# Kernel optimization log

Hardware: AMD Instinct MI355X
Metric: run time of the kernel (lower is better)

## Reference

```python
import jax, jax.numpy as jnp
import numpy as np

N, M = 30000, 32
VX, VY, VZ = 0.2, 0.2, 4.0
XOFF, YOFF, ZOFF = 0.1, -39.9, -1.0  # vx/2+pc_range[0], vy/2+pc_range[1], vz/2+pc_range[2]
EPS = 1e-3
H = 3  # num_heads, head_dim = 3 // 3 = 1


def setup_inputs() -> dict:
    key = jax.random.key(0)
    ks = jax.random.split(key, 13)
    features = jax.random.normal(ks[0], (N, M, 4), jnp.float32)
    num_points = jax.random.randint(ks[1], (N,), 1, M + 1, dtype=jnp.int32)
    coors = jax.random.randint(ks[2], (N, 4), 0, 352, dtype=jnp.int32)
    # PFN layer params (Linear 10->64 no bias, BN1d affine)
    pfn_w = jax.random.normal(ks[3], (10, 64), jnp.float32) * 0.1
    bn_gamma = jnp.ones((64,), jnp.float32)
    bn_beta = jnp.zeros((64,), jnp.float32)
    # PillarAttention: MHA on 3-dim coords, 3 heads of dim 1
    wq = jax.random.normal(ks[4], (3, 3), jnp.float32) * 0.5
    wk = jax.random.normal(ks[5], (3, 3), jnp.float32) * 0.5
    wv = jax.random.normal(ks[6], (3, 3), jnp.float32) * 0.5
    wo = jax.random.normal(ks[7], (3, 3), jnp.float32) * 0.5
    bq = jax.random.normal(ks[8], (3,), jnp.float32) * 0.02
    bk = jax.random.normal(ks[9], (3,), jnp.float32) * 0.02
    bv = jax.random.normal(ks[10], (3,), jnp.float32) * 0.02
    bo = jax.random.normal(ks[11], (3,), jnp.float32) * 0.02
    return dict(features=features, num_points=num_points, coors=coors,
                pfn_w=pfn_w, bn_gamma=bn_gamma, bn_beta=bn_beta,
                wq=wq, wk=wk, wv=wv, wo=wo, bq=bq, bk=bk, bv=bv, bo=bo)


def _pillar_attention(xyz, wq, wk, wv, wo, bq, bk, bv, bo):
    # xyz: (N, M, 3); 3 heads of dim 1 -> per-head score is an outer product
    q = xyz @ wq + bq  # (N, M, 3)
    k = xyz @ wk + bk
    v = xyz @ wv + bv
    # head_dim = 1 => scale = 1/sqrt(1) = 1
    scores = jnp.einsum('nih,njh->nhij', q, k)          # (N, H, M, M)
    attn = jax.nn.softmax(scores, axis=-1)
    out = jnp.einsum('nhij,njh->nih', attn, v)          # (N, M, 3)
    return out @ wo + bo


def reference(features, num_points, coors, pfn_w, bn_gamma, bn_beta,
              wq, wk, wv, wo, bq, bk, bv, bo):
    dtype = features.dtype
    xyz = features[:, :, :3]  # original coords (attn & cluster use these, pre in-place write)

    # PillarAttention on raw xyz, then max over feature dim
    feat_attn = _pillar_attention(xyz, wq, wk, wv, wo, bq, bk, bv, bo)  # (N, M, 3)
    max_attn = jnp.max(feat_attn, axis=-1, keepdims=True)              # (N, M, 1)

    npts = num_points.astype(dtype)[:, None, None]                      # (N,1,1)
    # cluster center offsets (uses original xyz)
    points_mean = jnp.sum(xyz, axis=1, keepdims=True) / npts
    f_cluster = xyz - points_mean                                       # (N, M, 3)

    # voxel center offsets; coors = [batch, z, y, x]
    cf = coors.astype(dtype)
    cx = cf[:, 3] * VX + XOFF
    cy = cf[:, 2] * VY + YOFF
    cz = cf[:, 1] * VZ + ZOFF
    f_center = jnp.stack([xyz[:, :, 0] - cx[:, None],
                          xyz[:, :, 1] - cy[:, None],
                          xyz[:, :, 2] - cz[:, None]], axis=-1)          # (N, M, 3)

    # legacy=True in-place bug: features[:, :, :3] becomes f_center before concat
    feats = jnp.concatenate([f_center, features[:, :, 3:], f_cluster, f_center], axis=-1)  # (N, M, 10)

    # mask out padded points
    mask = (jnp.arange(M)[None, :] < num_points[:, None]).astype(dtype)[:, :, None]
    feats = feats * mask

    # PFNLayer (last_vfe=True): Linear -> BN1d (train-mode stats over N*M) -> LeakyReLU
    x = feats @ pfn_w                                                    # (N, M, 64)
    mean = jnp.mean(x, axis=(0, 1))
    var = jnp.var(x, axis=(0, 1))
    x = (x - mean) * jax.lax.rsqrt(var + EPS) * bn_gamma + bn_beta
    x = jax.nn.leaky_relu(x, negative_slope=0.01)                        # (N, M, 64)

    # attention-weighted max pool fused with plain max pool
    fa = max_attn * x / jnp.sum(max_attn, axis=1, keepdims=True)
    fa = jnp.max(fa, axis=1, keepdims=True)                              # (N, 1, 64)
    fm = jnp.max(x, axis=1, keepdims=True)                               # (N, 1, 64)
    f = (fa + fm) * 0.5
    return f[:, 0, :]                                                    # (N, 64)
```

## Files before the change

### kernel.cpp

```cpp
#include <hip/hip_runtime.h>
#include <float.h>
#include <math.h>

constexpr int NP = 30000;
constexpr int M  = 32;
constexpr float VXc = 0.2f, VYc = 0.2f, VZc = 4.0f;
constexpr float XOFFc = 0.1f, YOFFc = -39.9f, ZOFFc = -1.0f;

__device__ __forceinline__ float wavesum64(float v) {
#pragma unroll
    for (int m = 32; m >= 1; m >>= 1) v += __shfl_xor(v, m, 64);
    return v;
}

__global__ __launch_bounds__(256) void stats_kernel(
    const float4* __restrict__ fp,
    const int*    __restrict__ num_points,
    const int*    __restrict__ coors,
    double*       __restrict__ Sout)
{
    float S[35];
#pragma unroll
    for (int k = 0; k < 35; ++k) S[k] = 0.f;

    int n = blockIdx.x * blockDim.x + threadIdx.x;
    if (n < NP) {
        int npts = num_points[n];
        int c1 = coors[4 * n + 1], c2 = coors[4 * n + 2], c3 = coors[4 * n + 3];
        float cx = (float)c3 * VXc + XOFFc;
        float cy = (float)c2 * VYc + YOFFc;
        float cz = (float)c1 * VZc + ZOFFc;
        const float4* p = fp + (size_t)n * M;

        float sx = 0.f, sy = 0.f, sz = 0.f;
        for (int i = 0; i < M; ++i) { float4 f = p[i]; sx += f.x; sy += f.y; sz += f.z; }
        float inv = 1.f / (float)npts;
        float mx = sx * inv, my = sy * inv, mz = sz * inv;

        for (int i = 0; i < npts; ++i) {
            float4 f = p[i];
            float u[7] = { f.x - cx, f.y - cy, f.z - cz, f.w,
                           f.x - mx, f.y - my, f.z - mz };
#pragma unroll
            for (int k = 0; k < 7; ++k) S[k] += u[k];
            int idx = 7;
#pragma unroll
            for (int k = 0; k < 7; ++k)
#pragma unroll
                for (int l = k; l < 7; ++l)
                    S[idx++] += u[k] * u[l];
        }
    }

#pragma unroll
    for (int k = 0; k < 35; ++k) S[k] = wavesum64(S[k]);

    __shared__ float part[4][35];
    int wid = threadIdx.x >> 6, ln = threadIdx.x & 63;
    if (ln == 0) {
#pragma unroll
        for (int k = 0; k < 35; ++k) part[wid][k] = S[k];
    }
    __syncthreads();
    if (threadIdx.x < 35) {
        float t = part[0][threadIdx.x] + part[1][threadIdx.x] +
                  part[2][threadIdx.x] + part[3][threadIdx.x];
        atomicAdd(&Sout[threadIdx.x], (double)t);
    }
}

__global__ __launch_bounds__(64) void affine_kernel(
    const double* __restrict__ S,
    const float*  __restrict__ pfn_w,
    const float*  __restrict__ gamma,
    const float*  __restrict__ beta,
    float*        __restrict__ AB)
{
    int c = threadIdx.x;
    double w7[7];
    w7[0] = (double)pfn_w[0 * 64 + c] + (double)pfn_w[7 * 64 + c];
    w7[1] = (double)pfn_w[1 * 64 + c] + (double)pfn_w[8 * 64 + c];
    w7[2] = (double)pfn_w[2 * 64 + c] + (double)pfn_w[9 * 64 + c];
    w7[3] = (double)pfn_w[3 * 64 + c];
    w7[4] = (double)pfn_w[4 * 64 + c];
    w7[5] = (double)pfn_w[5 * 64 + c];
    w7[6] = (double)pfn_w[6 * 64 + c];

    const double invNM = 1.0 / ((double)NP * (double)M);
    double mean = 0.0;
#pragma unroll
    for (int k = 0; k < 7; ++k) mean += S[k] * w7[k];
    mean *= invNM;

    double ex2 = 0.0;
    int idx = 7;
#pragma unroll
    for (int k = 0; k < 7; ++k)
#pragma unroll
        for (int l = k; l < 7; ++l) {
            double t = S[idx++] * w7[k] * w7[l];
            ex2 += (k == l) ? t : 2.0 * t;
        }
    ex2 *= invNM;

    double var = ex2 - mean * mean;
    double a = (double)gamma[c] / sqrt(var + 1e-3);
    AB[c]      = (float)a;
    AB[64 + c] = (float)((double)beta[c] - mean * a);
}

__global__ __launch_bounds__(64) void main_kernel(
    const float4* __restrict__ fp,
    const int*    __restrict__ num_points,
    const int*    __restrict__ coors,
    const float*  __restrict__ pfn_w,
    const float*  __restrict__ AB,
    const float*  __restrict__ wq, const float* __restrict__ wk,
    const float*  __restrict__ wv, const float* __restrict__ wo,
    const float*  __restrict__ bq, const float* __restrict__ bk,
    const float*  __restrict__ bv, const float* __restrict__ bo,
    float*        __restrict__ out)
{
    const int n    = blockIdx.x;
    const int lane = threadIdx.x;
    const int i    = lane & 31;

    __shared__ float k_s[3][32];
    __shared__ float v_s[3][32];
    __shared__ float u_s[32][7];
    __shared__ float r_s[32];

    const float4 f = fp[(size_t)n * M + i];

    float q[3], kk[3], vv[3];
#pragma unroll
    for (int h = 0; h < 3; ++h) {
        q[h]  = f.x * wq[0 * 3 + h] + f.y * wq[1 * 3 + h] + f.z * wq[2 * 3 + h] + bq[h];
        kk[h] = f.x * wk[0 * 3 + h] + f.y * wk[1 * 3 + h] + f.z * wk[2 * 3 + h] + bk[h];
        vv[h] = f.x * wv[0 * 3 + h] + f.y * wv[1 * 3 + h] + f.z * wv[2 * 3 + h] + bv[h];
    }
    if (lane < 32) {
#pragma unroll
        for (int h = 0; h < 3; ++h) { k_s[h][i] = kk[h]; v_s[h][i] = vv[h]; }
    }

    float sx = f.x, sy = f.y, sz = f.z;
    float kmx[3], kmn[3];
#pragma unroll
    for (int h = 0; h < 3; ++h) { kmx[h] = kk[h]; kmn[h] = kk[h]; }
#pragma unroll
    for (int m = 16; m >= 1; m >>= 1) {
        sx += __shfl_xor(sx, m, 32);
        sy += __shfl_xor(sy, m, 32);
        sz += __shfl_xor(sz, m, 32);
#pragma unroll
        for (int h = 0; h < 3; ++h) {
            kmx[h] = fmaxf(kmx[h], __shfl_xor(kmx[h], m, 32));
            kmn[h] = fminf(kmn[h], __shfl_xor(kmn[h], m, 32));
        }
    }
    __syncthreads();

    float o[3];
#pragma unroll
    for (int h = 0; h < 3; ++h) {
        const float qh = q[h];
        const float mrow = qh * (qh >= 0.f ? kmx[h] : kmn[h]);
        float den = 0.f, num = 0.f;
#pragma unroll
        for (int j = 0; j < 32; ++j) {
            float e = __expf(qh * k_s[h][j] - mrow);
            den += e;
            num += e * v_s[h][j];
        }
        o[h] = num / den;
    }
    float fa0 = o[0] * wo[0] + o[1] * wo[3] + o[2] * wo[6] + bo[0];
    float fa1 = o[0] * wo[1] + o[1] * wo[4] + o[2] * wo[7] + bo[1];
    float fa2 = o[0] * wo[2] + o[1] * wo[5] + o[2] * wo[8] + bo[2];
    float ma  = fmaxf(fa0, fmaxf(fa1, fa2));

    float sum_ma = ma;
#pragma unroll
    for (int m = 16; m >= 1; m >>= 1) sum_ma += __shfl_xor(sum_ma, m, 32);
    const float r = ma / sum_ma;

    const int npts = num_points[n];
    if (lane < 32) {
        r_s[i] = r;
        const float inv = 1.f / (float)npts;
        const float mx = sx * inv, my = sy * inv, mz = sz * inv;
        const int c1 = coors[4 * n + 1], c2 = coors[4 * n + 2], c3 = coors[4 * n + 3];
        const float cx = (float)c3 * VXc + XOFFc;
        const float cy = (float)c2 * VYc + YOFFc;
        const float cz = (float)c1 * VZc + ZOFFc;
        const bool valid = (i < npts);
        u_s[i][0] = valid ? f.x - cx : 0.f;
        u_s[i][1] = valid ? f.y - cy : 0.f;
        u_s[i][2] = valid ? f.z - cz : 0.f;
        u_s[i][3] = valid ? f.w      : 0.f;
        u_s[i][4] = valid ? f.x - mx : 0.f;
        u_s[i][5] = valid ? f.y - my : 0.f;
        u_s[i][6] = valid ? f.z - mz : 0.f;
    }
    __syncthreads();

    const int c = lane;
    float w7[7];
    w7[0] = pfn_w[0 * 64 + c] + pfn_w[7 * 64 + c];
    w7[1] = pfn_w[1 * 64 + c] + pfn_w[8 * 64 + c];
    w7[2] = pfn_w[2 * 64 + c] + pfn_w[9 * 64 + c];
    w7[3] = pfn_w[3 * 64 + c];
    w7[4] = pfn_w[4 * 64 + c];
    w7[5] = pfn_w[5 * 64 + c];
    w7[6] = pfn_w[6 * 64 + c];
    const float a = AB[c];
    const float b = AB[64 + c];

    float fm = -FLT_MAX, fav = -FLT_MAX;
#pragma unroll
    for (int ii = 0; ii < 32; ++ii) {
        float x = u_s[ii][0] * w7[0] + u_s[ii][1] * w7[1] + u_s[ii][2] * w7[2] +
                  u_s[ii][3] * w7[3] + u_s[ii][4] * w7[4] + u_s[ii][5] * w7[5] +
                  u_s[ii][6] * w7[6];
        float y = x * a + b;
        y = (y > 0.f) ? y : 0.01f * y;
        fm  = fmaxf(fm, y);
        fav = fmaxf(fav, r_s[ii] * y);
    }
    out[(size_t)n * 64 + c] = 0.5f * (fav + fm);
}

extern "C" void kernel_launch(void* const* d_in, const int* in_sizes, int n_in,
                              void* d_out, int out_size, void* d_ws, size_t ws_size,
                              hipStream_t stream) {
    const float4* feats  = (const float4*)d_in[0];
    const int*    npts   = (const int*)d_in[1];
    const int*    coors  = (const int*)d_in[2];
    const float*  pfn_w  = (const float*)d_in[3];
    const float*  gamma  = (const float*)d_in[4];
    const float*  beta   = (const float*)d_in[5];
    const float*  wq     = (const float*)d_in[6];
    const float*  wk     = (const float*)d_in[7];
    const float*  wv     = (const float*)d_in[8];
    const float*  wo     = (const float*)d_in[9];
    const float*  bq     = (const float*)d_in[10];
    const float*  bk     = (const float*)d_in[11];
    const float*  bv     = (const float*)d_in[12];
    const float*  bo     = (const float*)d_in[13];
    float*        out    = (float*)d_out;

    double* S  = (double*)d_ws;
    float*  AB = (float*)((char*)d_ws + 280);

    hipMemsetAsync(d_ws, 0, 280, stream);

    stats_kernel<<<(NP + 255) / 256, 256, 0, stream>>>(feats, npts, coors, S);
    affine_kernel<<<1, 64, 0, stream>>>(S, pfn_w, gamma, beta, AB);
    main_kernel<<<NP, 64, 0, stream>>>(feats, npts, coors, pfn_w, AB,
                                       wq, wk, wv, wo, bq, bk, bv, bo, out);
}
```

Baseline: 171.6 us.

## Use bf16 MFMA for PFN projection, point-parallel stats, four pillars per block

The stats kernel now assigns one point per thread in a grid-stride pattern and reduces pillar centroids with warp shuffles, replacing the serial per-pillar loops. The PFN 7->64 projection in the main kernel becomes two 32x32x16 bf16 MFMA instructions fed by prepacked bf16 weights. The main kernel also packs four pillars per 256-thread block and splits the attention inner loop across the two half-waves, using exp2. BF16 rounding of inputs and weights adds precision error relative to the fp32 reference.

```diff
diff --git a/kernel.cpp b/kernel.cpp
--- a/kernel.cpp
+++ b/kernel.cpp
@@ -7,10 +7,13 @@
 constexpr float VXc = 0.2f, VYc = 0.2f, VZc = 4.0f;
 constexpr float XOFFc = 0.1f, YOFFc = -39.9f, ZOFFc = -1.0f;
 
-__device__ __forceinline__ float wavesum64(float v) {
-#pragma unroll
-    for (int m = 32; m >= 1; m >>= 1) v += __shfl_xor(v, m, 64);
-    return v;
+typedef __attribute__((ext_vector_type(8)))  short bf16x8;
+typedef __attribute__((ext_vector_type(16))) float f32x16;
+
+__device__ __forceinline__ unsigned short f2bf(float x) {
+    unsigned int u = __builtin_bit_cast(unsigned int, x);
+    u = (u + 0x7fffu + ((u >> 16) & 1u)) >> 16;
+    return (unsigned short)u;
 }
 
 __global__ __launch_bounds__(256) void stats_kernel(
@@ -23,40 +26,58 @@
 #pragma unroll
     for (int k = 0; k < 35; ++k) S[k] = 0.f;
 
-    int n = blockIdx.x * blockDim.x + threadIdx.x;
-    if (n < NP) {
-        int npts = num_points[n];
-        int c1 = coors[4 * n + 1], c2 = coors[4 * n + 2], c3 = coors[4 * n + 3];
-        float cx = (float)c3 * VXc + XOFFc;
-        float cy = (float)c2 * VYc + YOFFc;
-        float cz = (float)c1 * VZc + ZOFFc;
-        const float4* p = fp + (size_t)n * M;
-
-        float sx = 0.f, sy = 0.f, sz = 0.f;
-        for (int i = 0; i < M; ++i) { float4 f = p[i]; sx += f.x; sy += f.y; sz += f.z; }
-        float inv = 1.f / (float)npts;
-        float mx = sx * inv, my = sy * inv, mz = sz * inv;
-
-        for (int i = 0; i < npts; ++i) {
-            float4 f = p[i];
-            float u[7] = { f.x - cx, f.y - cy, f.z - cz, f.w,
-                           f.x - mx, f.y - my, f.z - mz };
-#pragma unroll
-            for (int k = 0; k < 7; ++k) S[k] += u[k];
-            int idx = 7;
-#pragma unroll
-            for (int k = 0; k < 7; ++k)
-#pragma unroll
-                for (int l = k; l < 7; ++l)
-                    S[idx++] += u[k] * u[l];
-        }
-    }
-
-#pragma unroll
-    for (int k = 0; k < 35; ++k) S[k] = wavesum64(S[k]);
+    const int stride = gridDim.x * blockDim.x;
+    const int base   = blockIdx.x * blockDim.x + threadIdx.x;
+
+    for (int it = 0; it < 8; ++it) {
+        const int p = base + it * stride;
+        if (p >= NP * M) continue;
+        const int n = p >> 5;
+        const int i = p & 31;
+        const float4 f = fp[p];
+
+        float sx = f.x, sy = f.y, sz = f.z;
+#pragma unroll
+        for (int m = 16; m >= 1; m >>= 1) {
+            sx += __shfl_xor(sx, m, 32);
+            sy += __shfl_xor(sy, m, 32);
+            sz += __shfl_xor(sz, m, 32);
+        }
+        const int npts = num_points[n];
+        const float inv = 1.f / (float)npts;
+        const int c1 = coors[4 * n + 1], c2 = coors[4 * n + 2], c3 = coors[4 * n + 3];
+        const float cx = (float)c3 * VXc + XOFFc;
+        const float cy = (float)c2 * VYc + YOFFc;
+        const float cz = (float)c1 * VZc + ZOFFc;
+        const bool valid = (i < npts);
+
+        float u[7];
+        u[0] = valid ? f.x - cx : 0.f;
+        u[1] = valid ? f.y - cy : 0.f;
+        u[2] = valid ? f.z - cz : 0.f;
+        u[3] = valid ? f.w      : 0.f;
+        u[4] = valid ? f.x - sx * inv : 0.f;
+        u[5] = valid ? f.y - sy * inv : 0.f;
+        u[6] = valid ? f.z - sz * inv : 0.f;
+
+#pragma unroll
+        for (int k = 0; k < 7; ++k) S[k] += u[k];
+        int idx = 7;
+#pragma unroll
+        for (int k = 0; k < 7; ++k)
+#pragma unroll
+            for (int l = k; l < 7; ++l)
+                S[idx++] += u[k] * u[l];
+    }
+
+#pragma unroll
+    for (int k = 0; k < 35; ++k) {
+#pragma unroll
+        for (int m = 32; m >= 1; m >>= 1) S[k] += __shfl_xor(S[k], m, 64);
+    }
 
     __shared__ float part[4][35];
-    int wid = threadIdx.x >> 6, ln = threadIdx.x & 63;
+    const int wid = threadIdx.x >> 6, ln = threadIdx.x & 63;
     if (ln == 0) {
 #pragma unroll
         for (int k = 0; k < 35; ++k) part[wid][k] = S[k];
@@ -69,66 +90,94 @@
     }
 }
 
-__global__ __launch_bounds__(64) void affine_kernel(
+__global__ __launch_bounds__(128) void affine_kernel(
     const double* __restrict__ S,
     const float*  __restrict__ pfn_w,
     const float*  __restrict__ gamma,
     const float*  __restrict__ beta,
-    float*        __restrict__ AB)
+    float*        __restrict__ AB,
+    unsigned short* __restrict__ Wpk)
 {
-    int c = threadIdx.x;
-    double w7[7];
-    w7[0] = (double)pfn_w[0 * 64 + c] + (double)pfn_w[7 * 64 + c];
-    w7[1] = (double)pfn_w[1 * 64 + c] + (double)pfn_w[8 * 64 + c];
-    w7[2] = (double)pfn_w[2 * 64 + c] + (double)pfn_w[9 * 64 + c];
-    w7[3] = (double)pfn_w[3 * 64 + c];
-    w7[4] = (double)pfn_w[4 * 64 + c];
-    w7[5] = (double)pfn_w[5 * 64 + c];
-    w7[6] = (double)pfn_w[6 * 64 + c];
-
-    const double invNM = 1.0 / ((double)NP * (double)M);
-    double mean = 0.0;
-#pragma unroll
-    for (int k = 0; k < 7; ++k) mean += S[k] * w7[k];
-    mean *= invNM;
-
-    double ex2 = 0.0;
-    int idx = 7;
-#pragma unroll
-    for (int k = 0; k < 7; ++k)
-#pragma unroll
-        for (int l = k; l < 7; ++l) {
-            double t = S[idx++] * w7[k] * w7[l];
-            ex2 += (k == l) ? t : 2.0 * t;
-        }
-    ex2 *= invNM;
-
-    double var = ex2 - mean * mean;
-    double a = (double)gamma[c] / sqrt(var + 1e-3);
-    AB[c]      = (float)a;
-    AB[64 + c] = (float)((double)beta[c] - mean * a);
-}
-
-__global__ __launch_bounds__(64) void main_kernel(
+    const int tid = threadIdx.x;
+
+    if (tid < 64) {
+        const int c = tid;
+        double w7[7];
+        w7[0] = (double)pfn_w[0 * 64 + c] + (double)pfn_w[7 * 64 + c];
+        w7[1] = (double)pfn_w[1 * 64 + c] + (double)pfn_w[8 * 64 + c];
+        w7[2] = (double)pfn_w[2 * 64 + c] + (double)pfn_w[9 * 64 + c];
+        w7[3] = (double)pfn_w[3 * 64 + c];
+        w7[4] = (double)pfn_w[4 * 64 + c];
+        w7[5] = (double)pfn_w[5 * 64 + c];
+        w7[6] = (double)pfn_w[6 * 64 + c];
+
+        const double invNM = 1.0 / ((double)NP * (double)M);
+        double mean = 0.0;
+#pragma unroll
+        for (int k = 0; k < 7; ++k) mean += S[k] * w7[k];
+        mean *= invNM;
+
+        double ex2 = 0.0;
+        int idx = 7;
+#pragma unroll
+        for (int k = 0; k < 7; ++k)
+#pragma unroll
+            for (int l = k; l < 7; ++l) {
+                double t = S[idx++] * w7[k] * w7[l];
+                ex2 += (k == l) ? t : 2.0 * t;
+            }
+        ex2 *= invNM;
+
+        double var = ex2 - mean * mean;
+        double a = (double)gamma[c] / sqrt(var + 1e-3);
+        AB[c]      = (float)a;
+        AB[64 + c] = (float)((double)beta[c] - mean * a);
+    }
+
+    {
+        const int l = tid & 63;
+        const int t = tid >> 6;
+        const int half = l >> 5;
+        const int n = (l & 31) + 32 * t;
+        unsigned short v[8] = {0, 0, 0, 0, 0, 0, 0, 0};
+        if (half == 0) {
+            float w7[7];
+            w7[0] = pfn_w[0 * 64 + n] + pfn_w[7 * 64 + n];
+            w7[1] = pfn_w[1 * 64 + n] + pfn_w[8 * 64 + n];
+            w7[2] = pfn_w[2 * 64 + n] + pfn_w[9 * 64 + n];
+            w7[3] = pfn_w[3 * 64 + n];
+            w7[4] = pfn_w[4 * 64 + n];
+            w7[5] = pfn_w[5 * 64 + n];
+            w7[6] = pfn_w[6 * 64 + n];
+#pragma unroll
+            for (int j = 0; j < 7; ++j) v[j] = f2bf(w7[j]);
+        }
+#pragma unroll
+        for (int j = 0; j < 8; ++j) Wpk[tid * 8 + j] = v[j];
+    }
+}
+
+__global__ __launch_bounds__(256) void main_kernel(
     const float4* __restrict__ fp,
     const int*    __restrict__ num_points,
     const int*    __restrict__ coors,
-    const float*  __restrict__ pfn_w,
     const float*  __restrict__ AB,
+    const unsigned short* __restrict__ Wpk,
     const float*  __restrict__ wq, const float* __restrict__ wk,
     const float*  __restrict__ wv, const float* __restrict__ wo,
     const float*  __restrict__ bq, const float* __restrict__ bk,
     const float*  __restrict__ bv, const float* __restrict__ bo,
     float*        __restrict__ out)
 {
-    const int n    = blockIdx.x;
-    const int lane = threadIdx.x;
+    const int tid  = threadIdx.x;
+    const int pb   = tid >> 6;
+    const int lane = tid & 63;
     const int i    = lane & 31;
-
-    __shared__ float k_s[3][32];
-    __shared__ float v_s[3][32];
-    __shared__ float u_s[32][7];
-    __shared__ float r_s[32];
+    const int half = lane >> 5;
+    const int n    = blockIdx.x * 4 + pb;
+
+    __shared__ float2 kv_s[4][3][32];
+    __shared__ float  r_s[4][32];
 
     const float4 f = fp[(size_t)n * M + i];
 
@@ -139,9 +188,9 @@
         kk[h] = f.x * wk[0 * 3 + h] + f.y * wk[1 * 3 + h] + f.z * wk[2 * 3 + h] + bk[h];
         vv[h] = f.x * wv[0 * 3 + h] + f.y * wv[1 * 3 + h] + f.z * wv[2 * 3 + h] + bv[h];
     }
-    if (lane < 32) {
-#pragma unroll
-        for (int h = 0; h < 3; ++h) { k_s[h][i] = kk[h]; v_s[h][i] = vv[h]; }
+    if (half == 0) {
+#pragma unroll
+        for (int h = 0; h < 3; ++h) kv_s[pb][h][i] = make_float2(kk[h], vv[h]);
     }
 
     float sx = f.x, sy = f.y, sz = f.z;
@@ -161,74 +210,104 @@
     }
     __syncthreads();
 
-    float o[3];
+    const float LOG2E = 1.4426950408889634f;
+    float num[3], den[3];
+    const int j0 = half * 16;
 #pragma unroll
     for (int h = 0; h < 3; ++h) {
-        const float qh = q[h];
-        const float mrow = qh * (qh >= 0.f ? kmx[h] : kmn[h]);
-        float den = 0.f, num = 0.f;
-#pragma unroll
-        for (int j = 0; j < 32; ++j) {
-            float e = __expf(qh * k_s[h][j] - mrow);
-            den += e;
-            num += e * v_s[h][j];
-        }
-        o[h] = num / den;
-    }
-    float fa0 = o[0] * wo[0] + o[1] * wo[3] + o[2] * wo[6] + bo[0];
-    float fa1 = o[0] * wo[1] + o[1] * wo[4] + o[2] * wo[7] + bo[1];
-    float fa2 = o[0] * wo[2] + o[1] * wo[5] + o[2] * wo[8] + bo[2];
+        const float qh2  = q[h] * LOG2E;
+        const float mrow = qh2 * (q[h] >= 0.f ? kmx[h] : kmn[h]);
+        float d = 0.f, nu = 0.f;
+#pragma unroll
+        for (int jj = 0; jj < 16; ++jj) {
+            float2 kv = kv_s[pb][h][j0 + jj];
+            float e = exp2f(__builtin_fmaf(qh2, kv.x, -mrow));
+            d  += e;
+            nu += e * kv.y;
+        }
+        num[h] = nu; den[h] = d;
+    }
+#pragma unroll
+    for (int h = 0; h < 3; ++h) {
+        num[h] += __shfl_xor(num[h], 32, 64);
+        den[h] += __shfl_xor(den[h], 32, 64);
+    }
+    float o0 = num[0] / den[0], o1 = num[1] / den[1], o2 = num[2] / den[2];
+
+    float fa0 = o0 * wo[0] + o1 * wo[3] + o2 * wo[6] + bo[0];
+    float fa1 = o0 * wo[1] + o1 * wo[4] + o2 * wo[7] + bo[1];
+    float fa2 = o0 * wo[2] + o1 * wo[5] + o2 * wo[8] + bo[2];
     float ma  = fmaxf(fa0, fmaxf(fa1, fa2));
 
     float sum_ma = ma;
 #pragma unroll
     for (int m = 16; m >= 1; m >>= 1) sum_ma += __shfl_xor(sum_ma, m, 32);
     const float r = ma / sum_ma;
+    if (half == 0) r_s[pb][i] = r;
 
     const int npts = num_points[n];
-    if (lane < 32) {
-        r_s[i] = r;
-        const float inv = 1.f / (float)npts;
-        const float mx = sx * inv, my = sy * inv, mz = sz * inv;
-        const int c1 = coors[4 * n + 1], c2 = coors[4 * n + 2], c3 = coors[4 * n + 3];
-        const float cx = (float)c3 * VXc + XOFFc;
-        const float cy = (float)c2 * VYc + YOFFc;
-        const float cz = (float)c1 * VZc + ZOFFc;
-        const bool valid = (i < npts);
-        u_s[i][0] = valid ? f.x - cx : 0.f;
-        u_s[i][1] = valid ? f.y - cy : 0.f;
-        u_s[i][2] = valid ? f.z - cz : 0.f;
-        u_s[i][3] = valid ? f.w      : 0.f;
-        u_s[i][4] = valid ? f.x - mx : 0.f;
-        u_s[i][5] = valid ? f.y - my : 0.f;
-        u_s[i][6] = valid ? f.z - mz : 0.f;
-    }
+    const float inv = 1.f / (float)npts;
+    const int c1 = coors[4 * n + 1], c2 = coors[4 * n + 2], c3 = coors[4 * n + 3];
+    const float cx = (float)c3 * VXc + XOFFc;
+    const float cy = (float)c2 * VYc + YOFFc;
+    const float cz = (float)c1 * VZc + ZOFFc;
+    const bool valid = (i < npts);
+
+    float u[7];
+    u[0] = valid ? f.x - cx : 0.f;
+    u[1] = valid ? f.y - cy : 0.f;
+    u[2] = valid ? f.z - cz : 0.f;
+    u[3] = valid ? f.w      : 0.f;
+    u[4] = valid ? f.x - sx * inv : 0.f;
+    u[5] = valid ? f.y - sy * inv : 0.f;
+    u[6] = valid ? f.z - sz * inv : 0.f;
+
+    bf16x8 afr;
+#pragma unroll
+    for (int e = 0; e < 8; ++e) afr[e] = 0;
+    if (half == 0) {
+#pragma unroll
+        for (int e = 0; e < 7; ++e) afr[e] = (short)f2bf(u[e]);
+    }
+
+    const bf16x8 bf0 = *reinterpret_cast<const bf16x8*>(Wpk + (size_t)lane * 8);
+    const bf16x8 bf1 = *reinterpret_cast<const bf16x8*>(Wpk + (size_t)(64 + lane) * 8);
+
+    f32x16 acc0, acc1;
+#pragma unroll
+    for (int e = 0; e < 16; ++e) { acc0[e] = 0.f; acc1[e] = 0.f; }
+    acc0 = __builtin_amdgcn_mfma_f32_32x32x16_bf16(afr, bf0, acc0, 0, 0, 0);
+    acc1 = __builtin_amdgcn_mfma_f32_32x32x16_bf16(afr, bf1, acc1, 0, 0, 0);
+
     __syncthreads();
 
-    const int c = lane;
-    float w7[7];
-    w7[0] = pfn_w[0 * 64 + c] + pfn_w[7 * 64 + c];
-    w7[1] = pfn_w[1 * 64 + c] + pfn_w[8 * 64 + c];
-    w7[2] = pfn_w[2 * 64 + c] + pfn_w[9 * 64 + c];
-    w7[3] = pfn_w[3 * 64 + c];
-    w7[4] = pfn_w[4 * 64 + c];
-    w7[5] = pfn_w[5 * 64 + c];
-    w7[6] = pfn_w[6 * 64 + c];
-    const float a = AB[c];
-    const float b = AB[64 + c];
-
-    float fm = -FLT_MAX, fav = -FLT_MAX;
-#pragma unroll
-    for (int ii = 0; ii < 32; ++ii) {
-        float x = u_s[ii][0] * w7[0] + u_s[ii][1] * w7[1] + u_s[ii][2] * w7[2] +
-                  u_s[ii][3] * w7[3] + u_s[ii][4] * w7[4] + u_s[ii][5] * w7[5] +
-                  u_s[ii][6] * w7[6];
-        float y = x * a + b;
-        y = (y > 0.f) ? y : 0.01f * y;
-        fm  = fmaxf(fm, y);
-        fav = fmaxf(fav, r_s[ii] * y);
-    }
-    out[(size_t)n * 64 + c] = 0.5f * (fav + fm);
+    float rv[16];
+#pragma unroll
+    for (int rg = 0; rg < 16; ++rg) {
+        const int row = (rg & 3) + 8 * (rg >> 2) + 4 * half;
+        rv[rg] = r_s[pb][row];
+    }
+
+    float res[2];
+#pragma unroll
+    for (int t = 0; t < 2; ++t) {
+        const int c = (lane & 31) + 32 * t;
+        const float a = AB[c];
+        const float b = AB[64 + c];
+        float fm = -FLT_MAX, fav = -FLT_MAX;
+#pragma unroll
+        for (int rg = 0; rg < 16; ++rg) {
+            const float x = (t ? acc1[rg] : acc0[rg]);
+            float y = __builtin_fmaf(x, a, b);
+            y = fmaxf(y, 0.01f * y);
+            fm  = fmaxf(fm, y);
+            fav = fmaxf(fav, rv[rg] * y);
+        }
+        fm  = fmaxf(fm,  __shfl_xor(fm,  32, 64));
+        fav = fmaxf(fav, __shfl_xor(fav, 32, 64));
+        res[t] = 0.5f * (fav + fm);
+    }
+    out[(size_t)n * 64 + half * 32 + (lane & 31)] = res[half];
 }
 
 extern "C" void kernel_launch(void* const* d_in, const int* in_sizes, int n_in,
@@ -250,13 +329,14 @@
     const float*  bo     = (const float*)d_in[13];
     float*        out    = (float*)d_out;
 
-    double* S  = (double*)d_ws;
-    float*  AB = (float*)((char*)d_ws + 280);
+    double*         S   = (double*)d_ws;
+    float*          AB  = (float*)((char*)d_ws + 384);
+    unsigned short* Wpk = (unsigned short*)((char*)d_ws + 896);
 
     hipMemsetAsync(d_ws, 0, 280, stream);
 
-    stats_kernel<<<(NP + 255) / 256, 256, 0, stream>>>(feats, npts, coors, S);
-    affine_kernel<<<1, 64, 0, stream>>>(S, pfn_w, gamma, beta, AB);
-    main_kernel<<<NP, 64, 0, stream>>>(feats, npts, coors, pfn_w, AB,
-                                       wq, wk, wv, wo, bq, bk, bv, bo, out);
-}
+    stats_kernel<<<480, 256, 0, stream>>>(feats, npts, coors, S);
+    affine_kernel<<<1, 128, 0, stream>>>(S, pfn_w, gamma, beta, AB, Wpk);
+    main_kernel<<<NP / 4, 256, 0, stream>>>(feats, npts, coors, AB, Wpk,
+                                            wq, wk, wv, wo, bq, bk, bv, bo, out);
+}
```

Result: faster. 154.9 us (-9.8%).
